# Kernel tuning notes

Hardware: AMD Instinct MI355X
Metric: run time of the kernel (lower is better)

Reference implementation:

```python
import jax, jax.numpy as jnp
import numpy as np

N, V, J, NB = 512, 3889, 35, 20
PARENTS = np.array([0, 0, 1, 2, 3, 4, 5, 6, 7, 8, 9, 6, 11, 12, 13, 6, 15, 16, 17, 18,
                    16, 20, 21, 22, 23, 16, 25, 26, 27, 28, 29, 30, 16, 1, 1], dtype=np.int32)


def _rodrigues(theta):
    # theta: [M,3] axis-angle -> [M,3,3] rotation matrices (batch_rodrigues)
    angle = jnp.sqrt(jnp.sum(theta * theta, axis=1, keepdims=True) + 1e-8)  # [M,1]
    r = theta / angle                                                        # [M,3]
    c = jnp.cos(angle)[..., None]                                            # [M,1,1]
    s = jnp.sin(angle)[..., None]
    rr = r[:, :, None] * r[:, None, :]                                       # [M,3,3]
    z = jnp.zeros_like(r[:, 0])
    K = jnp.stack([z, -r[:, 2], r[:, 1],
                   r[:, 2], z, -r[:, 0],
                   -r[:, 1], r[:, 0], z], axis=1).reshape(-1, 3, 3)
    eye = jnp.eye(3, dtype=theta.dtype)
    return c * eye + (1.0 - c) * rr + s * K


def _make_A(R, t):
    # R: [N,3,3], t: [N,3] -> homogeneous [N,4,4]
    n = R.shape[0]
    top = jnp.concatenate([R, t[:, :, None]], axis=2)                        # [N,3,4]
    bot = jnp.broadcast_to(jnp.array([0.0, 0.0, 0.0, 1.0], R.dtype), (n, 1, 4))
    return jnp.concatenate([top, bot], axis=1)


def _global_rigid(Rs, Jp, scales, parents):
    # Rs: [N,35,3,3], Jp: [N,35,3], scales: [N,35,3] (diag scale factors)
    # diag(s_par)^-1 @ R @ diag(s) == R * s[col] / s_par[row]
    results = [_make_A(Rs[:, 0], Jp[:, 0])]
    for i in range(1, len(parents)):  # fixed 35-joint kinematic tree
        p = int(parents[i])
        j_here = Jp[:, i] - Jp[:, p]
        rot_new = Rs[:, i] * (scales[:, i][:, None, :] / scales[:, p][:, :, None])
        results.append(results[p] @ _make_A(rot_new, j_here))
    results = jnp.stack(results, axis=1)                                     # [N,35,4,4]
    new_J = results[:, :, :3, 3]
    # A = results - pad(results @ [J;0]) : subtract rest-pose bone from last column
    init_bone = jnp.einsum('njab,njb->nja', results[:, :, :, :3], Jp)        # [N,35,4]
    A = results - jnp.pad(init_bone[..., None], ((0, 0), (0, 0), (0, 0), (3, 0)))
    return new_J, A


def reference(beta, theta, betas_extra, deform_verts, trans, v_template,
              shapedirs, posedirs, J_regressor, weights, parents):
    par = np.asarray(jax.device_get(parents))
    n = beta.shape[0]
    v_shaped = v_template + deform_verts + (beta @ shapedirs).reshape(n, V, 3)
    Jp = jnp.einsum('nvc,vj->njc', v_shaped, J_regressor)                    # [N,35,3]
    Rs = _rodrigues(theta.reshape(n * J, 3)).reshape(n, J, 3, 3)
    pose_feature = (Rs[:, 1:] - jnp.eye(3, dtype=Rs.dtype)).reshape(n, 306)
    v_posed = (pose_feature @ posedirs).reshape(n, V, 3) + v_shaped
    scales = betas_extra.reshape(n, J, 3)
    _, A = _global_rigid(Rs, Jp, scales, par)
    T = jnp.einsum('vj,njab->nvab', weights, A)                              # [N,V,4,4] LBS blend
    v_h = jnp.concatenate([v_posed, jnp.ones((n, V, 1), v_posed.dtype)], axis=2)
    verts = jnp.einsum('nvab,nvb->nva', T, v_h)[..., :3] + trans[:, None, :]
    joints = jnp.einsum('nvc,vj->njc', verts, J_regressor)
    return verts, joints, Rs


def setup_inputs() -> dict:
    key = jax.random.key(0)
    ks = jax.random.split(key, 10)
    beta = 0.5 * jax.random.normal(ks[0], (N, NB), jnp.float32)
    theta = 0.2 * jax.random.normal(ks[1], (N, J * 3), jnp.float32)
    betas_extra = jnp.exp(0.1 * jax.random.normal(ks[2], (N, J * 3), jnp.float32))  # positive scales ~1
    deform_verts = 0.01 * jax.random.normal(ks[3], (N, V, 3), jnp.float32)
    trans = jax.random.normal(ks[4], (N, 3), jnp.float32)
    v_template = jax.random.normal(ks[5], (V, 3), jnp.float32)
    shapedirs = 0.01 * jax.random.normal(ks[6], (NB, V * 3), jnp.float32)
    posedirs = 0.01 * jax.random.normal(ks[7], (306, V * 3), jnp.float32)
    Jr = jax.random.uniform(ks[8], (V, J), jnp.float32)
    J_regressor = Jr / jnp.sum(Jr, axis=0, keepdims=True)   # columns sum to 1
    Wt = jax.random.uniform(ks[9], (V, J), jnp.float32)
    weights = Wt / jnp.sum(Wt, axis=1, keepdims=True)       # rows sum to 1 (skinning weights)
    return {"beta": beta, "theta": theta, "betas_extra": betas_extra,
            "deform_verts": deform_verts, "trans": trans, "v_template": v_template,
            "shapedirs": shapedirs, "posedirs": posedirs, "J_regressor": J_regressor,
            "weights": weights, "parents": jnp.asarray(PARENTS)}
```

## Files before the change

### kernel.cpp

```cpp
#include <hip/hip_runtime.h>

#define N_   512
#define V_   3889
#define V3   11667
#define J_   35
#define NB_  20
#define PF_K 306
#define KP2  352
#define KS2  11
#define EP2  11776
#define VP   3904
#define JRROWS 36
#define JCP  112
#define KB_  92
#define ECH  128
#define PLN  57344

typedef __attribute__((ext_vector_type(8))) short short8;
typedef __attribute__((ext_vector_type(4))) float f32x4;

__constant__ int c_parents[J_] = {0,0,1,2,3,4,5,6,7,8,9,6,11,12,13,6,15,16,17,18,
                                  16,20,21,22,23,16,25,26,27,28,29,30,16,1,1};

static __device__ __forceinline__ unsigned short f2bf(float x) {
  union { float f; unsigned int u; } v; v.f = x;
  unsigned int r = v.u + 0x7FFF + ((v.u >> 16) & 1);
  return (unsigned short)(r >> 16);
}

#define PA_JRT 549
#define PA_WTS 245
#define PA_PD  2024
#define PA_JB  644
#define PA_BLOCKS (PA_JRT + PA_WTS + PA_PD + PA_JB)
__global__ __launch_bounds__(256) void k_prep_a(
    const float* __restrict__ Jr,  const float* __restrict__ wts,
    const float* __restrict__ pd,  const float* __restrict__ sd,
    float* __restrict__ JrT, unsigned short* __restrict__ wtsB,
    unsigned short* __restrict__ pdT, unsigned short* __restrict__ JrBigT) {
  int b = blockIdx.x;
  int t = threadIdx.x;
  if (b < PA_JRT) {
    int idx = b * 256 + t;
    if (idx >= JRROWS * VP) return;
    int j = idx / VP, v = idx - j * VP;
    JrT[idx] = (j < J_ && v < V_) ? Jr[v * J_ + j] : 0.f;
  } else if (b < PA_JRT + PA_WTS) {
    int bb = b - PA_JRT;
    int v   = bb * 16 + (t >> 4);
    int jk0 = (t & 15) * 4;
    unsigned short pk[4];
#pragma unroll
    for (int i = 0; i < 4; ++i) {
      int j = jk0 + i;
      float x = (v < V_ && j < J_) ? wts[(size_t)v * J_ + j] : 0.f;
      pk[i] = f2bf(x);
    }
    *(unsigned long long*)(wtsB + (size_t)v * 64 + jk0) = *(unsigned long long*)pk;
  } else if (b < PA_JRT + PA_WTS + PA_PD) {
    int pp = b - (PA_JRT + PA_WTS);
    int ec = pp % 184, o4 = pp / 184;
    int e  = ec * 64 + (t & 63);
    int oc = o4 * 4 + (t >> 6);
    int k0 = oc * 8;
    bool ev = e < V3;
    union { unsigned short u[8]; short8 s; } pk;
#pragma unroll
    for (int ii = 0; ii < 8; ++ii) {
      int k = k0 + ii;
      float x = 0.f;
      if (ev && k < PF_K)            x = pd[(size_t)k * V3 + e];
      else if (ev && k < PF_K + NB_) x = sd[(size_t)(k - PF_K) * V3 + e];
      pk.u[ii] = f2bf(x);
    }
    *(short8*)(pdT + (size_t)e * KP2 + k0) = pk.s;
  } else {
    int o = (b - (PA_JRT + PA_WTS + PA_PD)) * 256 + t;
    int jc = o / 1472;
    int eo = (o - jc * 1472) * 8;
    int jj = jc / 3, cc = jc - jj * 3;
    union { unsigned short u[8]; short8 s; } pk;
#pragma unroll
    for (int i = 0; i < 8; ++i) {
      int e = eo + i;
      int v = e / 3, ce = e - v * 3;
      float x = (jc < 105 && e < V3 && ce == cc) ? Jr[v * J_ + jj] : 0.f;
      pk.u[i] = f2bf(x);
    }
    *(short8*)(JrBigT + (size_t)jc * EP2 + eo) = pk.s;
  }
}

#define JRJG 9
__global__ __launch_bounds__(512) void k_jp84(
    const float* __restrict__ JrT, const float* __restrict__ vt,
    const float* __restrict__ sd,  float* __restrict__ vtsdJr) {
  __shared__ float part[8][27];
  int b = blockIdx.x;
  int t = threadIdx.x;
  int lane = t & 63, w = t >> 6;
  int jg = w & 3, vh = w >> 2;
  int j0 = jg * JRJG;
  const float* jrb = JrT + (size_t)j0 * VP;

  int d = b >> 3, ch = b & 7;
  const float* s0 = (d == 0) ? vt : sd + (size_t)(d - 1) * V3;
  int c0 = ch * 2 + vh, cn = 1;
  bool tail = false;
  if (ch == 7 && vh == 1) { cn = 0; tail = true; }

  float acc[JRJG][3];
#pragma unroll
  for (int jj = 0; jj < JRJG; ++jj)
#pragma unroll
    for (int cc = 0; cc < 3; ++cc) acc[jj][cc] = 0.f;

  for (int i = 0; i < cn; ++i) {
    int v = (c0 + i) * 256 + lane * 4;
    f32x4 jr4[JRJG];
#pragma unroll
    for (int jj = 0; jj < JRJG; ++jj)
      jr4[jj] = *(const f32x4*)&jrb[(size_t)jj * VP + v];
    const float* dp = s0 + 3 * v;
    f32x4 da = *(const f32x4*)(dp);
    f32x4 db = *(const f32x4*)(dp + 4);
    f32x4 dc = *(const f32x4*)(dp + 8);
#pragma unroll
    for (int jj = 0; jj < JRJG; ++jj) {
      acc[jj][0] += jr4[jj][0]*da[0] + jr4[jj][1]*da[3] + jr4[jj][2]*db[2] + jr4[jj][3]*dc[1];
      acc[jj][1] += jr4[jj][0]*da[1] + jr4[jj][1]*db[0] + jr4[jj][2]*db[3] + jr4[jj][3]*dc[2];
      acc[jj][2] += jr4[jj][0]*da[2] + jr4[jj][1]*db[1] + jr4[jj][2]*dc[0] + jr4[jj][3]*dc[3];
    }
  }

  if (tail) {
    int v = 15 * 256 + lane * 4;
#pragma unroll
    for (int k = 0; k < 4; ++k) {
      int vv = v + k;
      if (vv < V_) {
        float dx = s0[3*vv], dy = s0[3*vv+1], dz = s0[3*vv+2];
#pragma unroll
        for (int jj = 0; jj < JRJG; ++jj) {
          float jr = jrb[(size_t)jj * VP + vv];
          acc[jj][0] += jr * dx; acc[jj][1] += jr * dy; acc[jj][2] += jr * dz;
        }
      }
    }
  }

#pragma unroll
  for (int jj = 0; jj < JRJG; ++jj)
#pragma unroll
    for (int cc = 0; cc < 3; ++cc) {
      float v = acc[jj][cc];
#pragma unroll
      for (int off = 32; off > 0; off >>= 1)
        v += __shfl_down(v, off, 64);
      if (lane == 0) part[w][jj * 3 + cc] = v;
    }
  __syncthreads();

  if (t < 108) {
    int g = t / 27, idx = t % 27;
    int j = g * JRJG + idx / 3;
    if (j < J_)
      atomicAdd(&vtsdJr[(b >> 3) * 105 + j * 3 + idx % 3],
                part[g][idx] + part[g + 4][idx]);
  }
}

__global__ __launch_bounds__(64) void k_jrgemm(
    const float* __restrict__ X, const unsigned short* __restrict__ JrBigT,
    float* __restrict__ planes) {
  int lane = threadIdx.x;
  int q = lane >> 4, c = lane & 15;
  int n = blockIdx.x * 16 + c;
  int kb = blockIdx.y;
  int e0 = kb * ECH;
  const float* xr = X + (size_t)n * V3;
  const short8* Ap = (const short8*)JrBigT;

  f32x4 acc[7];
#pragma unroll
  for (int tt = 0; tt < 7; ++tt) acc[tt] = (f32x4){0.f, 0.f, 0.f, 0.f};

  bool safe = (e0 + ECH <= V3);
  if (safe) {
#pragma unroll
    for (int ks = 0; ks < ECH / 32; ++ks) {
      int eb = e0 + ks * 32 + q * 8;
      f32x4 x0 = *(const f32x4*)(xr + eb);
      f32x4 x1 = *(const f32x4*)(xr + eb + 4);
      union { unsigned short u[8]; short8 s; } bq;
#pragma unroll
      for (int i = 0; i < 4; ++i) { bq.u[i] = f2bf(x0[i]); bq.u[4 + i] = f2bf(x1[i]); }
#pragma unroll
      for (int tt = 0; tt < 7; ++tt) {
        short8 a = Ap[((size_t)(tt * 16 + c) * EP2 + eb) >> 3];
        acc[tt] = __builtin_amdgcn_mfma_f32_16x16x32_bf16(a, bq.s, acc[tt], 0, 0, 0);
      }
    }
  } else {
#pragma unroll
    for (int ks = 0; ks < ECH / 32; ++ks) {
      int eb = e0 + ks * 32 + q * 8;
      union { unsigned short u[8]; short8 s; } bq;
#pragma unroll
      for (int i = 0; i < 8; ++i) {
        int e = eb + i;
        float x = (e < V3) ? xr[e] : 0.f;
        bq.u[i] = f2bf(x);
      }
#pragma unroll
      for (int tt = 0; tt < 7; ++tt) {
        short8 a = Ap[((size_t)(tt * 16 + c) * EP2 + eb) >> 3];
        acc[tt] = __builtin_amdgcn_mfma_f32_16x16x32_bf16(a, bq.s, acc[tt], 0, 0, 0);
      }
    }
  }

  float* pl = planes + (size_t)kb * PLN + (size_t)n * JCP;
#pragma unroll
  for (int tt = 0; tt < 7; ++tt)
    *(f32x4*)(pl + tt * 16 + q * 4) = acc[tt];
}

__global__ __launch_bounds__(256) void k_fold(
    const float* __restrict__ planes, float* __restrict__ dst) {
  int g = blockIdx.x * 256 + threadIdx.x;
  int n = g / 105, jc = g - n * 105;
  float s = 0.f;
  for (int kb = 0; kb < KB_; ++kb)
    s += planes[(size_t)kb * PLN + n * JCP + jc];
  dst[g] = s;
}

__global__ __launch_bounds__(256) void k_chain_rod(
    const float* __restrict__ theta, const float* __restrict__ JpRaw,
    const float* __restrict__ vtsdJr,
    const float* __restrict__ se,    const float* __restrict__ trans,
    const float* __restrict__ beta,
    float* __restrict__ Rs_out, unsigned short* __restrict__ pfA,
    unsigned short* __restrict__ AwB) {
  __shared__ float loc[4][J_][12];
  __shared__ float res[4][J_][12];
  __shared__ float Jp_s[4][J_][3];
  int t = threadIdx.x;
  int w = t >> 6, l = t & 63;
  int n = blockIdx.x * 4 + w;
  int mt = n >> 4, m = n & 15;

  float r[9];
  if (l < J_) {
    int j = l;
    const float* th = theta + n * (J_ * 3) + j * 3;
    float t0 = th[0], t1 = th[1], t2 = th[2];
    float angle = sqrtf(t0 * t0 + t1 * t1 + t2 * t2 + 1e-8f);
    float inv = 1.0f / angle;
    float r0 = t0 * inv, r1 = t1 * inv, r2 = t2 * inv;
    float s, c;
    sincosf(angle, &s, &c);
    float omc = 1.0f - c;
    r[0] = c + omc * r0 * r0;      r[1] = omc * r0 * r1 - s * r2;  r[2] = omc * r0 * r2 + s * r1;
    r[3] = omc * r1 * r0 + s * r2; r[4] = c + omc * r1 * r1;       r[5] = omc * r1 * r2 - s * r0;
    r[6] = omc * r2 * r0 - s * r1; r[7] = omc * r2 * r1 + s * r0;  r[8] = c + omc * r2 * r2;

    float* ro = Rs_out + (size_t)n * (J_ * 9) + j * 9;
#pragma unroll
    for (int k = 0; k < 9; ++k) ro[k] = r[k];
    if (j > 0) {
#pragma unroll
      for (int kk = 0; kk < 9; ++kk) {
        int k = (j - 1) * 9 + kk;
        float v = r[kk] - ((kk == 0 || kk == 4 || kk == 8) ? 1.0f : 0.0f);
        size_t idx = ((((size_t)mt * KS2 + (k >> 5)) * 4 + ((k >> 3) & 3)) * 16 + m) * 8 + (k & 7);
        pfA[idx] = f2bf(v);
      }
    }
    const float* bn = beta + n * NB_;
#pragma unroll
    for (int cc = 0; cc < 3; ++cc) {
      int jc = j * 3 + cc;
      float val = JpRaw[n * 105 + jc] + vtsdJr[jc];
#pragma unroll
      for (int bb = 0; bb < NB_; ++bb)
        val += bn[bb] * vtsdJr[(1 + bb) * 105 + jc];
      Jp_s[w][j][cc] = val;
    }
  } else {
    unsigned short* An = AwB + (size_t)n * 16 * 64 + l;
#pragma unroll
    for (int d = 0; d < 16; ++d) An[d * 64] = 0;
    if (l < 55) {
      int k = PF_K + (l - 35);
      size_t idx = ((((size_t)mt * KS2 + (k >> 5)) * 4 + ((k >> 3) & 3)) * 16 + m) * 8 + (k & 7);
      pfA[idx] = f2bf(beta[n * NB_ + (l - 35)]);
    } else {
      for (int k = PF_K + NB_ + (l - 55); k < KP2; k += 9) {
        size_t idx = ((((size_t)mt * KS2 + (k >> 5)) * 4 + ((k >> 3) & 3)) * 16 + m) * 8 + (k & 7);
        pfA[idx] = 0;
      }
    }
  }
  __syncthreads();

  if (l < J_) {
    int j = l;
    if (j == 0) {
#pragma unroll
      for (int rr = 0; rr < 3; ++rr) {
        loc[w][0][rr * 4 + 0] = r[rr * 3 + 0];
        loc[w][0][rr * 4 + 1] = r[rr * 3 + 1];
        loc[w][0][rr * 4 + 2] = r[rr * 3 + 2];
        loc[w][0][rr * 4 + 3] = Jp_s[w][0][rr];
      }
#pragma unroll
      for (int k = 0; k < 12; ++k) res[w][0][k] = loc[w][0][k];
    } else {
      int p = c_parents[j];
      float si[3], sp[3], jh[3];
#pragma unroll
      for (int cidx = 0; cidx < 3; ++cidx) {
        si[cidx] = se[n * 105 + j * 3 + cidx];
        sp[cidx] = se[n * 105 + p * 3 + cidx];
        jh[cidx] = Jp_s[w][j][cidx] - Jp_s[w][p][cidx];
      }
#pragma unroll
      for (int rr = 0; rr < 3; ++rr) {
        float invp = 1.0f / sp[rr];
        loc[w][j][rr * 4 + 0] = r[rr * 3 + 0] * si[0] * invp;
        loc[w][j][rr * 4 + 1] = r[rr * 3 + 1] * si[1] * invp;
        loc[w][j][rr * 4 + 2] = r[rr * 3 + 2] * si[2] * invp;
        loc[w][j][rr * 4 + 3] = jh[rr];
      }
    }
  }
  __syncthreads();

  for (int i = 1; i < J_; ++i) {
    if (l < 12) {
      int p = c_parents[i];
      int rr = l >> 2, cc = l & 3;
      float acc = (cc == 3) ? res[w][p][rr * 4 + 3] : 0.f;
#pragma unroll
      for (int k = 0; k < 3; ++k)
        acc += res[w][p][rr * 4 + k] * loc[w][i][k * 4 + cc];
      res[w][i][l] = acc;
    }
    __syncthreads();
  }

  if (l < J_) {
    int j = l;
    float jx = Jp_s[w][j][0];
    float jy = Jp_s[w][j][1];
    float jz = Jp_s[w][j][2];
    unsigned short* An = AwB + (size_t)n * 16 * 64 + j;
#pragma unroll
    for (int rr = 0; rr < 3; ++rr) {
      float a0 = res[w][j][rr * 4 + 0];
      float a1 = res[w][j][rr * 4 + 1];
      float a2 = res[w][j][rr * 4 + 2];
      float a3 = res[w][j][rr * 4 + 3] - (a0 * jx + a1 * jy + a2 * jz)
               + trans[n * 3 + rr];
      An[(rr * 4 + 0) * 64] = f2bf(a0);
      An[(rr * 4 + 1) * 64] = f2bf(a1);
      An[(rr * 4 + 2) * 64] = f2bf(a2);
      An[(rr * 4 + 3) * 64] = f2bf(a3);
    }
  }
}

#define LSTR 242
__global__ __launch_bounds__(256) void k_vposed_skin(
    const unsigned short* __restrict__ pfA, const unsigned short* __restrict__ pdT,
    const unsigned short* __restrict__ AwB, const unsigned short* __restrict__ wtsB,
    const float* __restrict__ vt, const float* __restrict__ deform,
    float* __restrict__ verts) {
  __shared__ float lds[64 * LSTR];
  int t = threadIdx.x;
  int wv = t >> 6, lane = t & 63;
  int q = lane >> 4, col = lane & 15;
  int bx = blockIdx.x, by = blockIdx.y;
  int mtg0 = by * 4;
  int ebase = bx * 240 + wv * 64;

  const short8* Ap = (const short8*)pfA;
  const short8* Bp = (const short8*)pdT;

  f32x4 acc[4][4];
#pragma unroll
  for (int mt = 0; mt < 4; ++mt)
#pragma unroll
    for (int et = 0; et < 4; ++et) acc[mt][et] = (f32x4){0.f, 0.f, 0.f, 0.f};

#pragma unroll
  for (int ks = 0; ks < KS2; ++ks) {
    short8 a[4];
#pragma unroll
    for (int mt = 0; mt < 4; ++mt)
      a[mt] = Ap[(((mtg0 + mt) * KS2 + ks) * 4 + q) * 16 + col];
    short8 b[4];
#pragma unroll
    for (int et = 0; et < 4; ++et)
      b[et] = Bp[(size_t)(ebase + et * 16 + col) * (KP2 / 8) + ks * 4 + q];
#pragma unroll
    for (int mt = 0; mt < 4; ++mt)
#pragma unroll
      for (int et = 0; et < 4; ++et)
        acc[mt][et] = __builtin_amdgcn_mfma_f32_16x16x32_bf16(a[mt], b[et], acc[mt][et], 0, 0, 0);
  }

#pragma unroll
  for (int et = 0; et < 4; ++et) {
    int e_loc = wv * 64 + et * 16 + col;
    int e = bx * 240 + e_loc;
    bool ev = (e < V3) && (e_loc < 240);
    float vte = ev ? vt[e] : 0.f;
#pragma unroll
    for (int mt = 0; mt < 4; ++mt) {
#pragma unroll
      for (int r = 0; r < 4; ++r) {
        int n_loc = mt * 16 + q * 4 + r;
        if (ev) {
          int n = by * 64 + n_loc;
          float df = deform[(size_t)n * V3 + e];
          lds[n_loc * LSTR + e_loc] = acc[mt][et][r] + vte + df;
        }
      }
    }
  }
  __syncthreads();

  short8 bw0[5], bw1[5];
#pragma unroll
  for (int v5 = 0; v5 < 5; ++v5) {
    int v = bx * 80 + v5 * 16 + col;
    const short8* Wp = (const short8*)(wtsB + (size_t)v * 64);
    bw0[v5] = Wp[q];
    bw1[v5] = Wp[4 + q];
  }
#pragma unroll 2
  for (int ni = 0; ni < 16; ++ni) {
    int n_loc = wv * 16 + ni;
    int n = by * 64 + n_loc;
    const short8* Aq = (const short8*)(AwB + ((size_t)n * 16 + col) * 64);
    short8 a0 = Aq[q];
    short8 a1 = Aq[4 + q];
#pragma unroll
    for (int v5 = 0; v5 < 5; ++v5) {
      f32x4 s = (f32x4){0.f, 0.f, 0.f, 0.f};
      s = __builtin_amdgcn_mfma_f32_16x16x32_bf16(a0, bw0[v5], s, 0, 0, 0);
      s = __builtin_amdgcn_mfma_f32_16x16x32_bf16(a1, bw1[v5], s, 0, 0, 0);
      int vl = v5 * 16 + col;
      int v = bx * 80 + vl;
      if (v < V_ && q < 3) {
        float x = lds[n_loc * LSTR + 3 * vl + 0];
        float y = lds[n_loc * LSTR + 3 * vl + 1];
        float z = lds[n_loc * LSTR + 3 * vl + 2];
        verts[(size_t)n * V3 + 3 * v + q] = s[0] * x + s[1] * y + s[2] * z + s[3];
      }
    }
  }
}

extern "C" void kernel_launch(void* const* d_in, const int* in_sizes, int n_in,
                              void* d_out, int out_size, void* d_ws, size_t ws_size,
                              hipStream_t stream) {
  const float* beta   = (const float*)d_in[0];
  const float* theta  = (const float*)d_in[1];
  const float* se     = (const float*)d_in[2];
  const float* deform = (const float*)d_in[3];
  const float* trans  = (const float*)d_in[4];
  const float* vt     = (const float*)d_in[5];
  const float* sd     = (const float*)d_in[6];
  const float* pd     = (const float*)d_in[7];
  const float* Jr     = (const float*)d_in[8];
  const float* wts    = (const float*)d_in[9];

  float* out    = (float*)d_out;
  float* verts  = out;
  float* joints = out + (size_t)N_ * V3;
  float* Rs     = joints + (size_t)N_ * 105;

  char* w = (char*)d_ws;
  unsigned short* pdT    = (unsigned short*)w;
  unsigned short* pfA    = (unsigned short*)(w + 8290304);
  float* planes = (float*)(w + 8650752);
  float* JpRawF = (float*)(w + 29753344);
  unsigned short* AwB    = (unsigned short*)(w + 29968384);
  float* JrT    = (float*)(w + 31016960);
  unsigned short* wtsB   = (unsigned short*)(w + 31579136);
  unsigned short* JrBigT = (unsigned short*)(w + 32080896);
  float* vtsdJr = (float*)(w + 34718720);

  hipMemsetAsync(vtsdJr, 0, 21 * 105 * sizeof(float), stream);
  k_prep_a<<<PA_BLOCKS, 256, 0, stream>>>(Jr, wts, pd, sd, JrT, wtsB, pdT, JrBigT);
  k_jp84<<<168, 512, 0, stream>>>(JrT, vt, sd, vtsdJr);
  k_jrgemm<<<dim3(32, KB_), 64, 0, stream>>>(deform, JrBigT, planes);
  k_fold<<<210, 256, 0, stream>>>(planes, JpRawF);
  k_chain_rod<<<N_ / 4, 256, 0, stream>>>(theta, JpRawF, vtsdJr, se, trans, beta,
                                          Rs, pfA, AwB);
  k_vposed_skin<<<dim3(49, 8), 256, 0, stream>>>(pfA, pdT, AwB, wtsB, vt, deform, verts);
  k_jrgemm<<<dim3(32, KB_), 64, 0, stream>>>(verts, JrBigT, planes);
  k_fold<<<210, 256, 0, stream>>>(planes, joints);
}
```

Measured before the change: 223.2 us.

## Rebalance split-K in joint regression, single-wave chain blocks, smaller skinning tiles

Cuts the joint-regression split-K count from 92 to 23 with 512-element chunks, shrinking the partial-plane buffer and the fold reduction. The kinematic chain kernel now runs one 64-thread wave per sample and drops block barriers, relying on in-wave ordering of shared memory. The posed-vertex/skinning kernel uses 32 samples per block instead of 64, doubling the grid and halving LDS and accumulators for better occupancy. The fewer, longer jrgemm blocks trade reduction traffic for less parallelism.

Result: no change. 224.1 us (+0.4%).

```diff
diff --git a/kernel.cpp b/kernel.cpp
--- a/kernel.cpp
+++ b/kernel.cpp
@@ -12,8 +12,8 @@
 #define VP   3904
 #define JRROWS 36
 #define JCP  112
-#define KB_  92
-#define ECH  128
+#define KB_  23
+#define ECH  512
 #define PLN  57344
 
 typedef __attribute__((ext_vector_type(8))) short short8;
@@ -231,24 +231,24 @@
   int g = blockIdx.x * 256 + threadIdx.x;
   int n = g / 105, jc = g - n * 105;
   float s = 0.f;
+#pragma unroll
   for (int kb = 0; kb < KB_; ++kb)
     s += planes[(size_t)kb * PLN + n * JCP + jc];
   dst[g] = s;
 }
 
-__global__ __launch_bounds__(256) void k_chain_rod(
+__global__ __launch_bounds__(64) void k_chain_rod(
     const float* __restrict__ theta, const float* __restrict__ JpRaw,
     const float* __restrict__ vtsdJr,
     const float* __restrict__ se,    const float* __restrict__ trans,
     const float* __restrict__ beta,
     float* __restrict__ Rs_out, unsigned short* __restrict__ pfA,
     unsigned short* __restrict__ AwB) {
-  __shared__ float loc[4][J_][12];
-  __shared__ float res[4][J_][12];
-  __shared__ float Jp_s[4][J_][3];
-  int t = threadIdx.x;
-  int w = t >> 6, l = t & 63;
-  int n = blockIdx.x * 4 + w;
+  __shared__ float loc[J_][12];
+  __shared__ float res[J_][12];
+  __shared__ float Jp_s[J_][3];
+  int l = threadIdx.x;
+  int n = blockIdx.x;
   int mt = n >> 4, m = n & 15;
 
   float r[9];
@@ -286,7 +286,7 @@
 #pragma unroll
       for (int bb = 0; bb < NB_; ++bb)
         val += bn[bb] * vtsdJr[(1 + bb) * 105 + jc];
-      Jp_s[w][j][cc] = val;
+      Jp_s[j][cc] = val;
     }
   } else {
     unsigned short* An = AwB + (size_t)n * 16 * 64 + l;
@@ -303,20 +303,19 @@
       }
     }
   }
-  __syncthreads();
 
   if (l < J_) {
     int j = l;
     if (j == 0) {
 #pragma unroll
       for (int rr = 0; rr < 3; ++rr) {
-        loc[w][0][rr * 4 + 0] = r[rr * 3 + 0];
-        loc[w][0][rr * 4 + 1] = r[rr * 3 + 1];
-        loc[w][0][rr * 4 + 2] = r[rr * 3 + 2];
-        loc[w][0][rr * 4 + 3] = Jp_s[w][0][rr];
-      }
-#pragma unroll
-      for (int k = 0; k < 12; ++k) res[w][0][k] = loc[w][0][k];
+        loc[0][rr * 4 + 0] = r[rr * 3 + 0];
+        loc[0][rr * 4 + 1] = r[rr * 3 + 1];
+        loc[0][rr * 4 + 2] = r[rr * 3 + 2];
+        loc[0][rr * 4 + 3] = Jp_s[0][rr];
+      }
+#pragma unroll
+      for (int k = 0; k < 12; ++k) res[0][k] = loc[0][k];
     } else {
       int p = c_parents[j];
       float si[3], sp[3], jh[3];
@@ -324,45 +323,43 @@
       for (int cidx = 0; cidx < 3; ++cidx) {
         si[cidx] = se[n * 105 + j * 3 + cidx];
         sp[cidx] = se[n * 105 + p * 3 + cidx];
-        jh[cidx] = Jp_s[w][j][cidx] - Jp_s[w][p][cidx];
+        jh[cidx] = Jp_s[j][cidx] - Jp_s[p][cidx];
       }
 #pragma unroll
       for (int rr = 0; rr < 3; ++rr) {
         float invp = 1.0f / sp[rr];
-        loc[w][j][rr * 4 + 0] = r[rr * 3 + 0] * si[0] * invp;
-        loc[w][j][rr * 4 + 1] = r[rr * 3 + 1] * si[1] * invp;
-        loc[w][j][rr * 4 + 2] = r[rr * 3 + 2] * si[2] * invp;
-        loc[w][j][rr * 4 + 3] = jh[rr];
-      }
-    }
-  }
-  __syncthreads();
+        loc[j][rr * 4 + 0] = r[rr * 3 + 0] * si[0] * invp;
+        loc[j][rr * 4 + 1] = r[rr * 3 + 1] * si[1] * invp;
+        loc[j][rr * 4 + 2] = r[rr * 3 + 2] * si[2] * invp;
+        loc[j][rr * 4 + 3] = jh[rr];
+      }
+    }
+  }
 
   for (int i = 1; i < J_; ++i) {
     if (l < 12) {
       int p = c_parents[i];
       int rr = l >> 2, cc = l & 3;
-      float acc = (cc == 3) ? res[w][p][rr * 4 + 3] : 0.f;
+      float acc = (cc == 3) ? res[p][rr * 4 + 3] : 0.f;
 #pragma unroll
       for (int k = 0; k < 3; ++k)
-        acc += res[w][p][rr * 4 + k] * loc[w][i][k * 4 + cc];
-      res[w][i][l] = acc;
-    }
-    __syncthreads();
+        acc += res[p][rr * 4 + k] * loc[i][k * 4 + cc];
+      res[i][l] = acc;
+    }
   }
 
   if (l < J_) {
     int j = l;
-    float jx = Jp_s[w][j][0];
-    float jy = Jp_s[w][j][1];
-    float jz = Jp_s[w][j][2];
+    float jx = Jp_s[j][0];
+    float jy = Jp_s[j][1];
+    float jz = Jp_s[j][2];
     unsigned short* An = AwB + (size_t)n * 16 * 64 + j;
 #pragma unroll
     for (int rr = 0; rr < 3; ++rr) {
-      float a0 = res[w][j][rr * 4 + 0];
-      float a1 = res[w][j][rr * 4 + 1];
-      float a2 = res[w][j][rr * 4 + 2];
-      float a3 = res[w][j][rr * 4 + 3] - (a0 * jx + a1 * jy + a2 * jz)
+      float a0 = res[j][rr * 4 + 0];
+      float a1 = res[j][rr * 4 + 1];
+      float a2 = res[j][rr * 4 + 2];
+      float a3 = res[j][rr * 4 + 3] - (a0 * jx + a1 * jy + a2 * jz)
                + trans[n * 3 + rr];
       An[(rr * 4 + 0) * 64] = f2bf(a0);
       An[(rr * 4 + 1) * 64] = f2bf(a1);
@@ -378,35 +375,35 @@
     const unsigned short* __restrict__ AwB, const unsigned short* __restrict__ wtsB,
     const float* __restrict__ vt, const float* __restrict__ deform,
     float* __restrict__ verts) {
-  __shared__ float lds[64 * LSTR];
+  __shared__ float lds[32 * LSTR];
   int t = threadIdx.x;
   int wv = t >> 6, lane = t & 63;
   int q = lane >> 4, col = lane & 15;
   int bx = blockIdx.x, by = blockIdx.y;
-  int mtg0 = by * 4;
+  int mtg0 = by * 2;
   int ebase = bx * 240 + wv * 64;
 
   const short8* Ap = (const short8*)pfA;
   const short8* Bp = (const short8*)pdT;
 
-  f32x4 acc[4][4];
-#pragma unroll
-  for (int mt = 0; mt < 4; ++mt)
+  f32x4 acc[2][4];
+#pragma unroll
+  for (int mt = 0; mt < 2; ++mt)
 #pragma unroll
     for (int et = 0; et < 4; ++et) acc[mt][et] = (f32x4){0.f, 0.f, 0.f, 0.f};
 
 #pragma unroll
   for (int ks = 0; ks < KS2; ++ks) {
-    short8 a[4];
-#pragma unroll
-    for (int mt = 0; mt < 4; ++mt)
+    short8 a[2];
+#pragma unroll
+    for (int mt = 0; mt < 2; ++mt)
       a[mt] = Ap[(((mtg0 + mt) * KS2 + ks) * 4 + q) * 16 + col];
     short8 b[4];
 #pragma unroll
     for (int et = 0; et < 4; ++et)
       b[et] = Bp[(size_t)(ebase + et * 16 + col) * (KP2 / 8) + ks * 4 + q];
 #pragma unroll
-    for (int mt = 0; mt < 4; ++mt)
+    for (int mt = 0; mt < 2; ++mt)
 #pragma unroll
       for (int et = 0; et < 4; ++et)
         acc[mt][et] = __builtin_amdgcn_mfma_f32_16x16x32_bf16(a[mt], b[et], acc[mt][et], 0, 0, 0);
@@ -419,12 +416,12 @@
     bool ev = (e < V3) && (e_loc < 240);
     float vte = ev ? vt[e] : 0.f;
 #pragma unroll
-    for (int mt = 0; mt < 4; ++mt) {
+    for (int mt = 0; mt < 2; ++mt) {
 #pragma unroll
       for (int r = 0; r < 4; ++r) {
         int n_loc = mt * 16 + q * 4 + r;
         if (ev) {
-          int n = by * 64 + n_loc;
+          int n = by * 32 + n_loc;
           float df = deform[(size_t)n * V3 + e];
           lds[n_loc * LSTR + e_loc] = acc[mt][et][r] + vte + df;
         }
@@ -442,9 +439,9 @@
     bw1[v5] = Wp[4 + q];
   }
 #pragma unroll 2
-  for (int ni = 0; ni < 16; ++ni) {
-    int n_loc = wv * 16 + ni;
-    int n = by * 64 + n_loc;
+  for (int ni = 0; ni < 8; ++ni) {
+    int n_loc = wv * 8 + ni;
+    int n = by * 32 + n_loc;
     const short8* Aq = (const short8*)(AwB + ((size_t)n * 16 + col) * 64);
     short8 a0 = Aq[q];
     short8 a1 = Aq[4 + q];
@@ -488,21 +485,21 @@
   unsigned short* pdT    = (unsigned short*)w;
   unsigned short* pfA    = (unsigned short*)(w + 8290304);
   float* planes = (float*)(w + 8650752);
-  float* JpRawF = (float*)(w + 29753344);
-  unsigned short* AwB    = (unsigned short*)(w + 29968384);
-  float* JrT    = (float*)(w + 31016960);
-  unsigned short* wtsB   = (unsigned short*)(w + 31579136);
-  unsigned short* JrBigT = (unsigned short*)(w + 32080896);
-  float* vtsdJr = (float*)(w + 34718720);
+  float* JpRawF = (float*)(w + 13926400);
+  unsigned short* AwB    = (unsigned short*)(w + 14141440);
+  float* JrT    = (float*)(w + 15190016);
+  unsigned short* wtsB   = (unsigned short*)(w + 15752192);
+  unsigned short* JrBigT = (unsigned short*)(w + 16253952);
+  float* vtsdJr = (float*)(w + 18891776);
 
   hipMemsetAsync(vtsdJr, 0, 21 * 105 * sizeof(float), stream);
   k_prep_a<<<PA_BLOCKS, 256, 0, stream>>>(Jr, wts, pd, sd, JrT, wtsB, pdT, JrBigT);
   k_jp84<<<168, 512, 0, stream>>>(JrT, vt, sd, vtsdJr);
   k_jrgemm<<<dim3(32, KB_), 64, 0, stream>>>(deform, JrBigT, planes);
   k_fold<<<210, 256, 0, stream>>>(planes, JpRawF);
-  k_chain_rod<<<N_ / 4, 256, 0, stream>>>(theta, JpRawF, vtsdJr, se, trans, beta,
-                                          Rs, pfA, AwB);
-  k_vposed_skin<<<dim3(49, 8), 256, 0, stream>>>(pfA, pdT, AwB, wtsB, vt, deform, verts);
+  k_chain_rod<<<N_, 64, 0, stream>>>(theta, JpRawF, vtsdJr, se, trans, beta,
+                                     Rs, pfA, AwB);
+  k_vposed_skin<<<dim3(49, 16), 256, 0, stream>>>(pfA, pdT, AwB, wtsB, vt, deform, verts);
   k_jrgemm<<<dim3(32, KB_), 64, 0, stream>>>(verts, JrBigT, planes);
   k_fold<<<210, 256, 0, stream>>>(planes, joints);
 }
```
